# Kernel optimization log

Measured on AMD Instinct MI355X. Metric: run time of the kernel, lower is better.

Reference implementation:

```python
import jax, jax.numpy as jnp
import numpy as np

NEG = float(-2**32 + 1)
LN_EPS = 1e-5

def setup_inputs() -> dict:
    key = jax.random.key(0)
    ks = jax.random.split(key, 10)
    B, Sq, Sk, D = 8, 1024, 1024, 1024
    memory = jax.random.normal(ks[0], (B, Sk, D), jnp.float32)
    decoder_input = jax.random.normal(ks[1], (B, Sq, D), jnp.float32)
    query_mask = jax.random.uniform(ks[2], (B, Sq), jnp.float32)
    Wk = jax.random.normal(ks[3], (D, D), jnp.float32) * 0.02
    Wv = jax.random.normal(ks[4], (D, D), jnp.float32) * 0.02
    Wq = jax.random.normal(ks[5], (D, D), jnp.float32) * 0.02
    Wf = jax.random.normal(ks[6], (2 * D, D), jnp.float32) * 0.02
    bf = jnp.zeros((D,), jnp.float32)
    gamma = jnp.ones((D,), jnp.float32)
    beta = jnp.zeros((D,), jnp.float32)
    mask = jax.random.randint(ks[7], (B, Sq, Sk), 0, 2) == 1
    return dict(memory=memory, decoder_input=decoder_input, query_mask=query_mask,
                Wk=Wk, Wv=Wv, Wq=Wq, Wf=Wf, bf=bf, gamma=gamma, beta=beta, mask=mask)

def reference(memory, decoder_input, query_mask, Wk, Wv, Wq, Wf, bf, gamma, beta, mask):
    B, Sk, D = memory.shape
    Sq = decoder_input.shape[1]
    h = 8
    dh = D // h
    # projections (no bias), split heads -> [h, B, S, dh]
    K = (memory @ Wk).reshape(B, Sk, h, dh).transpose(2, 0, 1, 3)
    V = (memory @ Wv).reshape(B, Sk, h, dh).transpose(2, 0, 1, 3)
    Q = (decoder_input @ Wq).reshape(B, Sq, h, dh).transpose(2, 0, 1, 3)
    # scores [h, B, Sq, Sk]
    attn = jnp.einsum('hbqd,hbkd->hbqk', Q, K) / jnp.sqrt(jnp.float32(dh))
    attn = jnp.where(mask[None], NEG, attn)
    attn = jax.nn.softmax(attn, axis=-1)
    # non-standard post-softmax query-mask multiply
    attn = attn * query_mask[None, :, :, None]
    x = jnp.einsum('hbqk,hbkd->hbqd', attn, V)      # [h,B,Sq,dh]
    x = x.transpose(1, 2, 0, 3).reshape(B, Sq, D)    # concat heads
    x = jnp.concatenate([decoder_input, x], axis=-1)  # [B,Sq,2D]
    x = x @ Wf + bf
    x = x + decoder_input
    # LayerNorm
    mu = jnp.mean(x, axis=-1, keepdims=True)
    var = jnp.var(x, axis=-1, keepdims=True)
    x = (x - mu) * jax.lax.rsqrt(var + LN_EPS) * gamma + beta
    attns = attn.reshape(h * B, Sq, Sk)  # match torch layout [h*B,Sq,Sk]
    return x, attns
```

## Files before the change

kernel.cpp:

```cpp
#include <hip/hip_runtime.h>
#include <hip/hip_bf16.h>
#include <stdint.h>

typedef __attribute__((ext_vector_type(4))) float  floatx4;
typedef __attribute__((ext_vector_type(8))) short  shortx8;

__device__ __forceinline__ unsigned short f2bf(float f) {
    unsigned int u = __builtin_bit_cast(unsigned int, f);
    u += 0x7FFFu + ((u >> 16) & 1u);
    return (unsigned short)(u >> 16);
}
__device__ __forceinline__ float bf2f(unsigned short h) {
    unsigned int u = (unsigned int)h << 16;
    return __builtin_bit_cast(float, u);
}

__device__ __forceinline__ uint4 pack8(float4 a, float4 b) {
    uint4 r;
    r.x = (unsigned)f2bf(a.x) | ((unsigned)f2bf(a.y) << 16);
    r.y = (unsigned)f2bf(a.z) | ((unsigned)f2bf(a.w) << 16);
    r.z = (unsigned)f2bf(b.x) | ((unsigned)f2bf(b.y) << 16);
    r.w = (unsigned)f2bf(b.z) | ((unsigned)f2bf(b.w) << 16);
    return r;
}

__device__ __forceinline__ void gload16(const ushort* g, ushort* l) {
    __builtin_amdgcn_global_load_lds(
        (const __attribute__((address_space(1))) unsigned int*)g,
        (__attribute__((address_space(3))) unsigned int*)l, 16, 0, 0);
}

__global__ __launch_bounds__(256) void cast_both(const float* __restrict__ mem,
                                                 const float* __restrict__ dec,
                                                 ushort* __restrict__ mem_bf,
                                                 ushort* __restrict__ concat) {
    if (blockIdx.x < 4096) {
        long long i = ((long long)blockIdx.x * 256 + threadIdx.x) * 8;
        const float4* p = (const float4*)(mem + i);
        *(uint4*)(mem_bf + i) = pack8(p[0], p[1]);
    } else {
        long long i = ((long long)(blockIdx.x - 4096) * 256 + threadIdx.x) * 8;
        long long r = i >> 10, c = i & 1023;
        const float4* p = (const float4*)(dec + i);
        *(uint4*)(concat + r * 2048 + c) = pack8(p[0], p[1]);
    }
}

__global__ __launch_bounds__(256) void wtrans(const float* __restrict__ W,
                                              ushort* __restrict__ WT, int K, int N) {
    __shared__ float t[32][33];
    int tx = threadIdx.x, ty = threadIdx.y;
    int bx = blockIdx.x * 32;
    int by = blockIdx.y * 32;
    #pragma unroll
    for (int i = 0; i < 4; i++)
        t[ty + 8 * i][tx] = W[(size_t)(by + ty + 8 * i) * N + bx + tx];
    __syncthreads();
    #pragma unroll
    for (int i = 0; i < 4; i++)
        WT[(size_t)(bx + ty + 8 * i) * K + by + tx] = f2bf(t[tx][ty + 8 * i]);
}

__global__ __launch_bounds__(256) void wtrans3(const float* __restrict__ W0,
                                               const float* __restrict__ W1,
                                               const float* __restrict__ W2,
                                               ushort* __restrict__ T0,
                                               ushort* __restrict__ T1,
                                               ushort* __restrict__ T2) {
    __shared__ float t[32][33];
    const float* W = blockIdx.z == 0 ? W0 : (blockIdx.z == 1 ? W1 : W2);
    ushort* WT     = blockIdx.z == 0 ? T0 : (blockIdx.z == 1 ? T1 : T2);
    int tx = threadIdx.x, ty = threadIdx.y;
    int bx = blockIdx.x * 32;
    int by = blockIdx.y * 32;
    #pragma unroll
    for (int i = 0; i < 4; i++)
        t[ty + 8 * i][tx] = W[(size_t)(by + ty + 8 * i) * 1024 + bx + tx];
    __syncthreads();
    #pragma unroll
    for (int i = 0; i < 4; i++)
        WT[(size_t)(bx + ty + 8 * i) * 1024 + by + tx] = f2bf(t[tx][ty + 8 * i]);
}

__global__ __launch_bounds__(256) void vtrans(const ushort* __restrict__ V,
                                              ushort* __restrict__ VT) {
    __shared__ ushort t[32][33];
    int tx = threadIdx.x, ty = threadIdx.y;
    int bk = blockIdx.x * 32;
    int bd = blockIdx.y * 32;
    int z = blockIdx.z;
    int b = z >> 3, h = z & 7;
    #pragma unroll
    for (int i = 0; i < 4; i++)
        t[ty + 8 * i][tx] = V[((size_t)(b * 1024 + bk + ty + 8 * i)) * 1024 + h * 128 + bd + tx];
    __syncthreads();
    #pragma unroll
    for (int i = 0; i < 4; i++)
        VT[((size_t)((h * 8 + b) * 128 + bd + ty + 8 * i)) * 1024 + bk + tx] = t[tx][ty + 8 * i];
}

template <typename TC>
__global__ __launch_bounds__(256) void gemm_bt(
    const ushort* __restrict__ A, const ushort* __restrict__ Bt, TC* __restrict__ C,
    int K, int lda, int ldb, int ldc) {
    __shared__ ushort As[128 * 64];
    __shared__ ushort Bs[128 * 64];

    int tid = threadIdx.x;
    int bm = blockIdx.y * 128, bn = blockIdx.x * 128;
    int l = tid & 63, wid = tid >> 6;
    int l16 = l & 15, quad = l >> 4;
    int wm = (wid & 1) * 64, wn = (wid >> 1) * 64;

    int srow = tid >> 3;
    int scol = (tid & 7) * 8;

    floatx4 acc[4][4];
    #pragma unroll
    for (int i = 0; i < 4; i++)
        #pragma unroll
        for (int j = 0; j < 4; j++)
            acc[i][j] = {0.0f, 0.0f, 0.0f, 0.0f};

    for (int kt = 0; kt < K; kt += 64) {
        #pragma unroll
        for (int it = 0; it < 4; it++) {
            int row = it * 32 + srow;
            gload16(A + (size_t)(bm + row) * lda + kt + scol, &As[row * 64 + scol]);
            gload16(Bt + (size_t)(bn + row) * ldb + kt + scol, &Bs[row * 64 + scol]);
        }
        __syncthreads();
        #pragma unroll
        for (int kk = 0; kk < 64; kk += 32) {
            shortx8 af[4], bfr[4];
            #pragma unroll
            for (int i = 0; i < 4; i++)
                af[i] = *(const shortx8*)&As[(wm + i * 16 + l16) * 64 + kk + quad * 8];
            #pragma unroll
            for (int j = 0; j < 4; j++)
                bfr[j] = *(const shortx8*)&Bs[(wn + j * 16 + l16) * 64 + kk + quad * 8];
            #pragma unroll
            for (int i = 0; i < 4; i++)
                #pragma unroll
                for (int j = 0; j < 4; j++)
                    acc[i][j] = __builtin_amdgcn_mfma_f32_16x16x32_bf16(af[i], bfr[j], acc[i][j], 0, 0, 0);
        }
        __syncthreads();
    }

    #pragma unroll
    for (int i = 0; i < 4; i++) {
        #pragma unroll
        for (int j = 0; j < 4; j++) {
            int row0 = bm + wm + i * 16 + quad * 4;
            int col = bn + wn + j * 16 + l16;
            #pragma unroll
            for (int r = 0; r < 4; r++) {
                float v = acc[i][j][r];
                size_t idx = (size_t)(row0 + r) * ldc + col;
                if constexpr (__is_same(TC, float)) C[idx] = v;
                else C[idx] = f2bf(v);
            }
        }
    }
}

__global__ __launch_bounds__(256) void fused_attn(
    const ushort* __restrict__ Qp, const ushort* __restrict__ Kp,
    const ushort* __restrict__ VT, const int* __restrict__ mask,
    const float* __restrict__ qmask, float* __restrict__ attns,
    ushort* __restrict__ concat) {
    __shared__ ushort Qs[16 * 136];
    __shared__ ushort Ss[16 * 1032];
    __shared__ float rowpart[16][17];
    __shared__ float scale_s[16];

    const int b = blockIdx.z, h = blockIdx.y, q0 = blockIdx.x * 16;
    const int tid = threadIdx.x;
    const int w = tid >> 6, l = tid & 63;
    const int l16 = l & 15, quad = l >> 4;
    const float sc = 0.08838834764831845f;

    {
        int row = tid >> 4, col = (tid & 15) * 8;
        *(uint4*)&Qs[row * 136 + col] =
            *(const uint4*)(Qp + (size_t)(b * 1024 + q0 + row) * 1024 + h * 128 + col);
    }
    __syncthreads();

    shortx8 af[4];
    #pragma unroll
    for (int kk = 0; kk < 4; kk++)
        af[kk] = *(const shortx8*)&Qs[l16 * 136 + kk * 32 + quad * 8];

    const size_t mbase = (size_t)b * 1048576 + (size_t)q0 * 1024;
    for (int c = 0; c < 16; ++c) {
        int k0 = c * 64 + w * 16;
        const ushort* Kr = Kp + (size_t)(b * 1024 + k0 + l16) * 1024 + h * 128 + quad * 8;
        floatx4 acc = {0.0f, 0.0f, 0.0f, 0.0f};
        #pragma unroll
        for (int kk = 0; kk < 4; ++kk)
            acc = __builtin_amdgcn_mfma_f32_16x16x32_bf16(af[kk], *(const shortx8*)(Kr + kk * 32), acc, 0, 0, 0);
        #pragma unroll
        for (int r = 0; r < 4; ++r) {
            int q = quad * 4 + r;
            int m = mask[mbase + (size_t)q * 1024 + k0 + l16];
            float v = m ? 0.0f : __expf(acc[r] * sc);
            Ss[q * 1032 + k0 + l16] = f2bf(v);
        }
    }
    __syncthreads();

    {
        int row = tid >> 4, cs = (tid & 15) * 64;
        float s = 0.0f;
        #pragma unroll
        for (int i = 0; i < 8; ++i) {
            shortx8 v = *(const shortx8*)&Ss[row * 1032 + cs + i * 8];
            #pragma unroll
            for (int j = 0; j < 8; ++j) s += bf2f((unsigned short)v[j]);
        }
        rowpart[row][tid & 15] = s;
    }
    __syncthreads();
    if (tid < 16) {
        float s = 0.0f;
        #pragma unroll
        for (int i = 0; i < 16; ++i) s += rowpart[tid][i];
        scale_s[tid] = qmask[b * 1024 + q0 + tid] / s;
    }
    __syncthreads();

    {
        int row = tid >> 4;
        float scl = scale_s[row];
        float* arow = attns + ((size_t)((h * 8 + b) * 1024 + q0 + row)) * 1024;
        int c0 = (tid & 15) * 4;
        #pragma unroll
        for (int j = 0; j < 16; ++j) {
            int c = c0 + j * 64;
            ushort4 v = *(const ushort4*)&Ss[row * 1032 + c];
            floatx4 o;
            o.x = bf2f(v.x) * scl;
            o.y = bf2f(v.y) * scl;
            o.z = bf2f(v.z) * scl;
            o.w = bf2f(v.w) * scl;
            __builtin_nontemporal_store(o, (floatx4*)(arow + c));
        }
    }

    const size_t vrow0 = (size_t)((h * 8 + b) * 128 + w * 32);
    floatx4 oacc[2] = {{0.0f, 0.0f, 0.0f, 0.0f}, {0.0f, 0.0f, 0.0f, 0.0f}};
    for (int c = 0; c < 16; ++c) {
        #pragma unroll
        for (int ks = 0; ks < 2; ++ks) {
            shortx8 a = *(const shortx8*)&Ss[l16 * 1032 + c * 64 + ks * 32 + quad * 8];
            #pragma unroll
            for (int j = 0; j < 2; ++j) {
                const ushort* vp = VT + (vrow0 + j * 16 + l16) * 1024 + c * 64 + ks * 32 + quad * 8;
                oacc[j] = __builtin_amdgcn_mfma_f32_16x16x32_bf16(a, *(const shortx8*)vp, oacc[j], 0, 0, 0);
            }
        }
    }
    #pragma unroll
    for (int j = 0; j < 2; ++j) {
        #pragma unroll
        for (int r = 0; r < 4; ++r) {
            int q = quad * 4 + r;
            int d = w * 32 + j * 16 + l16;
            float v = oacc[j][r] * scale_s[q];
            concat[(size_t)(b * 1024 + q0 + q) * 2048 + 1024 + h * 128 + d] = f2bf(v);
        }
    }
}

__global__ __launch_bounds__(256) void ln_out(const float* __restrict__ ffn,
                                              const float* __restrict__ dec,
                                              const float* __restrict__ bfv,
                                              const float* __restrict__ gamma,
                                              const float* __restrict__ beta,
                                              float* __restrict__ out) {
    __shared__ float sb[8];
    int row = blockIdx.x, tid = threadIdx.x;
    int c = tid * 4;
    size_t base = (size_t)row * 1024 + c;
    float4 x = *(const float4*)(ffn + base);
    float4 d = *(const float4*)(dec + base);
    float4 bb = *(const float4*)(bfv + c);
    x.x += d.x + bb.x; x.y += d.y + bb.y; x.z += d.z + bb.z; x.w += d.w + bb.w;

    float s = x.x + x.y + x.z + x.w;
    float s2 = x.x * x.x + x.y * x.y + x.z * x.z + x.w * x.w;
    #pragma unroll
    for (int o = 32; o; o >>= 1) {
        s += __shfl_down(s, o, 64);
        s2 += __shfl_down(s2, o, 64);
    }
    if ((tid & 63) == 0) { sb[tid >> 6] = s; sb[4 + (tid >> 6)] = s2; }
    __syncthreads();
    s = sb[0] + sb[1] + sb[2] + sb[3];
    s2 = sb[4] + sb[5] + sb[6] + sb[7];
    float mu = s * (1.0f / 1024.0f);
    float var = s2 * (1.0f / 1024.0f) - mu * mu;
    float rs = rsqrtf(var + 1e-5f);

    float4 g = *(const float4*)(gamma + c);
    float4 be = *(const float4*)(beta + c);
    float4 o4;
    o4.x = (x.x - mu) * rs * g.x + be.x;
    o4.y = (x.y - mu) * rs * g.y + be.y;
    o4.z = (x.z - mu) * rs * g.z + be.z;
    o4.w = (x.w - mu) * rs * g.w + be.w;
    *(float4*)(out + base) = o4;
}

extern "C" void kernel_launch(void* const* d_in, const int* in_sizes, int n_in,
                              void* d_out, int out_size, void* d_ws, size_t ws_size,
                              hipStream_t stream) {
    const float* memory  = (const float*)d_in[0];
    const float* decoder = (const float*)d_in[1];
    const float* qmask   = (const float*)d_in[2];
    const float* Wk      = (const float*)d_in[3];
    const float* Wv      = (const float*)d_in[4];
    const float* Wq      = (const float*)d_in[5];
    const float* Wf      = (const float*)d_in[6];
    const float* bfv     = (const float*)d_in[7];
    const float* gamma   = (const float*)d_in[8];
    const float* beta    = (const float*)d_in[9];
    const int*   mask    = (const int*)d_in[10];

    float* xout  = (float*)d_out;
    float* attns = xout + 8388608LL;

    char* w = (char*)d_ws;
    ushort* mem_bf = (ushort*)(w + 0);
    ushort* Kp     = (ushort*)(w + (16LL << 20));
    float*  ffn    = (float*)(w + 0);
    ushort* Qp     = (ushort*)(w + (32LL << 20));
    ushort* Vp     = (ushort*)(w + (48LL << 20));
    ushort* VT     = (ushort*)(w + (64LL << 20));
    ushort* concat = (ushort*)(w + (80LL << 20));
    ushort* WkT    = (ushort*)(w + (112LL << 20));
    ushort* WvT    = (ushort*)(w + (114LL << 20));
    ushort* WqT    = (ushort*)(w + (116LL << 20));
    ushort* WfT    = (ushort*)(w + (118LL << 20));

    cast_both<<<8192, 256, 0, stream>>>(memory, decoder, mem_bf, concat);
    wtrans3<<<dim3(32, 32, 3), dim3(32, 8), 0, stream>>>(Wk, Wv, Wq, WkT, WvT, WqT);
    wtrans<<<dim3(32, 64), dim3(32, 8), 0, stream>>>(Wf, WfT, 2048, 1024);
    gemm_bt<ushort><<<dim3(8, 64), 256, 0, stream>>>(mem_bf, WkT, Kp, 1024, 1024, 1024, 1024);
    gemm_bt<ushort><<<dim3(8, 64), 256, 0, stream>>>(mem_bf, WvT, Vp, 1024, 1024, 1024, 1024);
    gemm_bt<ushort><<<dim3(8, 64), 256, 0, stream>>>(concat, WqT, Qp, 1024, 2048, 1024, 1024);
    vtrans<<<dim3(32, 4, 64), dim3(32, 8), 0, stream>>>(Vp, VT);
    fused_attn<<<dim3(64, 8, 8), 256, 0, stream>>>(Qp, Kp, VT, mask, qmask, attns, concat);
    gemm_bt<float><<<dim3(8, 64), 256, 0, stream>>>(concat, WfT, ffn, 2048, 2048, 2048, 1024);
    ln_out<<<8192, 256, 0, stream>>>(ffn, decoder, bfv, gamma, beta, xout);
}
```

Baseline: 774.1 us.

## Bit-pack attention mask, merge projection GEMMs, split-K FFN, prefetch K/V in attention

Packs the int32 mask into 64-bit ballot words once, so each attention block reads 16 bits per row pair instead of re-reading int32 mask entries per head. The three projection GEMMs are merged into one launch, and the FFN GEMM is split along K into two partial outputs that LayerNorm sums, doubling the grid for more parallelism. Inside attention, K and V fragments are register-prefetched one chunk ahead, row sums are accumulated during exponentiation instead of by a separate shared-memory pass, and MFMA priority is raised. This costs an extra pack kernel plus an extra fp32 partial buffer read in LayerNorm.

```diff
diff --git a/kernel.cpp b/kernel.cpp
--- a/kernel.cpp
+++ b/kernel.cpp
@@ -46,6 +46,18 @@
     }
 }
 
+__global__ __launch_bounds__(256) void pack_mask(const int* __restrict__ mask,
+                                                 unsigned long long* __restrict__ mb) {
+    int gw = (blockIdx.x * 256 + threadIdx.x) >> 6;
+    int l = threadIdx.x & 63;
+    #pragma unroll
+    for (int i = 0; i < 16; ++i) {
+        size_t widx = (size_t)gw * 16 + i;
+        unsigned long long m = __ballot(mask[widx * 64 + l] != 0);
+        if (l == 0) mb[widx] = m;
+    }
+}
+
 __global__ __launch_bounds__(256) void wtrans(const float* __restrict__ W,
                                               ushort* __restrict__ WT, int K, int N) {
     __shared__ float t[32][33];
@@ -100,18 +112,15 @@
 }
 
 template <typename TC>
-__global__ __launch_bounds__(256) void gemm_bt(
-    const ushort* __restrict__ A, const ushort* __restrict__ Bt, TC* __restrict__ C,
-    int K, int lda, int ldb, int ldc) {
-    __shared__ ushort As[128 * 64];
-    __shared__ ushort Bs[128 * 64];
-
+__device__ __forceinline__ void gemm_core(ushort* As, ushort* Bs,
+                                          const ushort* __restrict__ A,
+                                          const ushort* __restrict__ Bt, TC* __restrict__ C,
+                                          int kbeg, int kend, int lda, int ldb, int ldc,
+                                          int bm, int bn) {
     int tid = threadIdx.x;
-    int bm = blockIdx.y * 128, bn = blockIdx.x * 128;
     int l = tid & 63, wid = tid >> 6;
     int l16 = l & 15, quad = l >> 4;
     int wm = (wid & 1) * 64, wn = (wid >> 1) * 64;
-
     int srow = tid >> 3;
     int scol = (tid & 7) * 8;
 
@@ -122,7 +131,7 @@
         for (int j = 0; j < 4; j++)
             acc[i][j] = {0.0f, 0.0f, 0.0f, 0.0f};
 
-    for (int kt = 0; kt < K; kt += 64) {
+    for (int kt = kbeg; kt < kend; kt += 64) {
         #pragma unroll
         for (int it = 0; it < 4; it++) {
             int row = it * 32 + srow;
@@ -165,14 +174,41 @@
     }
 }
 
-__global__ __launch_bounds__(256) void fused_attn(
+__global__ __launch_bounds__(256) void gemm_proj3(
+    const ushort* __restrict__ mem_bf, const ushort* __restrict__ concat,
+    const ushort* __restrict__ WkT, const ushort* __restrict__ WvT,
+    const ushort* __restrict__ WqT,
+    ushort* __restrict__ Kp, ushort* __restrict__ Vp, ushort* __restrict__ Qp) {
+    __shared__ ushort As[128 * 64];
+    __shared__ ushort Bs[128 * 64];
+    const ushort* A; const ushort* Bt; ushort* C; int lda;
+    if (blockIdx.z == 0)      { A = mem_bf; Bt = WkT; C = Kp; lda = 1024; }
+    else if (blockIdx.z == 1) { A = mem_bf; Bt = WvT; C = Vp; lda = 1024; }
+    else                      { A = concat; Bt = WqT; C = Qp; lda = 2048; }
+    gemm_core<ushort>(As, Bs, A, Bt, C, 0, 1024, lda, 1024, 1024,
+                      blockIdx.y * 128, blockIdx.x * 128);
+}
+
+__global__ __launch_bounds__(256) void gemm_ffn(
+    const ushort* __restrict__ concat, const ushort* __restrict__ WfT,
+    float* __restrict__ ffn0, float* __restrict__ ffn1) {
+    __shared__ ushort As[128 * 64];
+    __shared__ ushort Bs[128 * 64];
+    int z = blockIdx.z;
+    gemm_core<float>(As, Bs, concat, WfT, z ? ffn1 : ffn0,
+                     z * 1024, z * 1024 + 1024, 2048, 2048, 1024,
+                     blockIdx.y * 128, blockIdx.x * 128);
+}
+
+__global__ __launch_bounds__(256, 4) void fused_attn(
     const ushort* __restrict__ Qp, const ushort* __restrict__ Kp,
-    const ushort* __restrict__ VT, const int* __restrict__ mask,
+    const ushort* __restrict__ VT, const unsigned long long* __restrict__ mb,
     const float* __restrict__ qmask, float* __restrict__ attns,
     ushort* __restrict__ concat) {
     __shared__ ushort Qs[16 * 136];
     __shared__ ushort Ss[16 * 1032];
-    __shared__ float rowpart[16][17];
+    __shared__ unsigned Ms[16][34];
+    __shared__ float rowpart[16][5];
     __shared__ float scale_s[16];
 
     const int b = blockIdx.z, h = blockIdx.y, q0 = blockIdx.x * 16;
@@ -185,6 +221,10 @@
         int row = tid >> 4, col = (tid & 15) * 8;
         *(uint4*)&Qs[row * 136 + col] =
             *(const uint4*)(Qp + (size_t)(b * 1024 + q0 + row) * 1024 + h * 128 + col);
+        int pr = tid & 15;
+        uint2 mv = ((const uint2*)mb)[(size_t)(b * 1024 + q0 + row) * 16 + pr];
+        Ms[row][pr * 2] = mv.x;
+        Ms[row][pr * 2 + 1] = mv.y;
     }
     __syncthreads();
 
@@ -193,40 +233,54 @@
     for (int kk = 0; kk < 4; kk++)
         af[kk] = *(const shortx8*)&Qs[l16 * 136 + kk * 32 + quad * 8];
 
-    const size_t mbase = (size_t)b * 1048576 + (size_t)q0 * 1024;
+    const ushort* Kb = Kp + (size_t)(b * 1024 + w * 16 + l16) * 1024 + h * 128 + quad * 8;
+    shortx8 kf0 = *(const shortx8*)(Kb + 0);
+    shortx8 kf1 = *(const shortx8*)(Kb + 32);
+    shortx8 kf2 = *(const shortx8*)(Kb + 64);
+    shortx8 kf3 = *(const shortx8*)(Kb + 96);
+    float ssum[4] = {0.0f, 0.0f, 0.0f, 0.0f};
+    const int bp64 = w * 16 + l16;
+    const int wsel = bp64 >> 5, bitp = bp64 & 31;
     for (int c = 0; c < 16; ++c) {
+        int cn = c < 15 ? c + 1 : c;
+        const ushort* Kn = Kb + (size_t)cn * 65536;
+        shortx8 kn0 = *(const shortx8*)(Kn + 0);
+        shortx8 kn1 = *(const shortx8*)(Kn + 32);
+        shortx8 kn2 = *(const shortx8*)(Kn + 64);
+        shortx8 kn3 = *(const shortx8*)(Kn + 96);
+        floatx4 acc = {0.0f, 0.0f, 0.0f, 0.0f};
+        __builtin_amdgcn_s_setprio(1);
+        acc = __builtin_amdgcn_mfma_f32_16x16x32_bf16(af[0], kf0, acc, 0, 0, 0);
+        acc = __builtin_amdgcn_mfma_f32_16x16x32_bf16(af[1], kf1, acc, 0, 0, 0);
+        acc = __builtin_amdgcn_mfma_f32_16x16x32_bf16(af[2], kf2, acc, 0, 0, 0);
+        acc = __builtin_amdgcn_mfma_f32_16x16x32_bf16(af[3], kf3, acc, 0, 0, 0);
+        __builtin_amdgcn_s_setprio(0);
         int k0 = c * 64 + w * 16;
-        const ushort* Kr = Kp + (size_t)(b * 1024 + k0 + l16) * 1024 + h * 128 + quad * 8;
-        floatx4 acc = {0.0f, 0.0f, 0.0f, 0.0f};
-        #pragma unroll
-        for (int kk = 0; kk < 4; ++kk)
-            acc = __builtin_amdgcn_mfma_f32_16x16x32_bf16(af[kk], *(const shortx8*)(Kr + kk * 32), acc, 0, 0, 0);
         #pragma unroll
         for (int r = 0; r < 4; ++r) {
             int q = quad * 4 + r;
-            int m = mask[mbase + (size_t)q * 1024 + k0 + l16];
-            float v = m ? 0.0f : __expf(acc[r] * sc);
+            unsigned wv = Ms[q][c * 2 + wsel];
+            float v = ((wv >> bitp) & 1u) ? 0.0f : __expf(acc[r] * sc);
+            ssum[r] += v;
             Ss[q * 1032 + k0 + l16] = f2bf(v);
         }
-    }
-    __syncthreads();
-
-    {
-        int row = tid >> 4, cs = (tid & 15) * 64;
-        float s = 0.0f;
-        #pragma unroll
-        for (int i = 0; i < 8; ++i) {
-            shortx8 v = *(const shortx8*)&Ss[row * 1032 + cs + i * 8];
-            #pragma unroll
-            for (int j = 0; j < 8; ++j) s += bf2f((unsigned short)v[j]);
-        }
-        rowpart[row][tid & 15] = s;
+        kf0 = kn0; kf1 = kn1; kf2 = kn2; kf3 = kn3;
+    }
+
+    #pragma unroll
+    for (int r = 0; r < 4; ++r) {
+        float s = ssum[r];
+        #pragma unroll
+        for (int off = 1; off < 16; off <<= 1) s += __shfl_xor(s, off, 16);
+        ssum[r] = s;
+    }
+    if (l16 == 0) {
+        #pragma unroll
+        for (int r = 0; r < 4; ++r) rowpart[quad * 4 + r][w] = ssum[r];
     }
     __syncthreads();
     if (tid < 16) {
-        float s = 0.0f;
-        #pragma unroll
-        for (int i = 0; i < 16; ++i) s += rowpart[tid][i];
+        float s = rowpart[tid][0] + rowpart[tid][1] + rowpart[tid][2] + rowpart[tid][3];
         scale_s[tid] = qmask[b * 1024 + q0 + tid] / s;
     }
     __syncthreads();
@@ -250,31 +304,42 @@
     }
 
     const size_t vrow0 = (size_t)((h * 8 + b) * 128 + w * 32);
-    floatx4 oacc[2] = {{0.0f, 0.0f, 0.0f, 0.0f}, {0.0f, 0.0f, 0.0f, 0.0f}};
+    const ushort* Vb0 = VT + (vrow0 + l16) * 1024 + quad * 8;
+    const ushort* Vb1 = VT + (vrow0 + 16 + l16) * 1024 + quad * 8;
+    shortx8 v00 = *(const shortx8*)(Vb0);
+    shortx8 v01 = *(const shortx8*)(Vb1);
+    shortx8 v10 = *(const shortx8*)(Vb0 + 32);
+    shortx8 v11 = *(const shortx8*)(Vb1 + 32);
+    floatx4 o0 = {0.0f, 0.0f, 0.0f, 0.0f}, o1 = {0.0f, 0.0f, 0.0f, 0.0f};
     for (int c = 0; c < 16; ++c) {
-        #pragma unroll
-        for (int ks = 0; ks < 2; ++ks) {
-            shortx8 a = *(const shortx8*)&Ss[l16 * 1032 + c * 64 + ks * 32 + quad * 8];
-            #pragma unroll
-            for (int j = 0; j < 2; ++j) {
-                const ushort* vp = VT + (vrow0 + j * 16 + l16) * 1024 + c * 64 + ks * 32 + quad * 8;
-                oacc[j] = __builtin_amdgcn_mfma_f32_16x16x32_bf16(a, *(const shortx8*)vp, oacc[j], 0, 0, 0);
-            }
-        }
-    }
-    #pragma unroll
-    for (int j = 0; j < 2; ++j) {
-        #pragma unroll
-        for (int r = 0; r < 4; ++r) {
-            int q = quad * 4 + r;
-            int d = w * 32 + j * 16 + l16;
-            float v = oacc[j][r] * scale_s[q];
-            concat[(size_t)(b * 1024 + q0 + q) * 2048 + 1024 + h * 128 + d] = f2bf(v);
-        }
-    }
-}
-
-__global__ __launch_bounds__(256) void ln_out(const float* __restrict__ ffn,
+        int cn = c < 15 ? c + 1 : c;
+        shortx8 n00 = *(const shortx8*)(Vb0 + cn * 64);
+        shortx8 n01 = *(const shortx8*)(Vb1 + cn * 64);
+        shortx8 n10 = *(const shortx8*)(Vb0 + cn * 64 + 32);
+        shortx8 n11 = *(const shortx8*)(Vb1 + cn * 64 + 32);
+        shortx8 pa0 = *(const shortx8*)&Ss[l16 * 1032 + c * 64 + quad * 8];
+        shortx8 pa1 = *(const shortx8*)&Ss[l16 * 1032 + c * 64 + 32 + quad * 8];
+        __builtin_amdgcn_s_setprio(1);
+        o0 = __builtin_amdgcn_mfma_f32_16x16x32_bf16(pa0, v00, o0, 0, 0, 0);
+        o1 = __builtin_amdgcn_mfma_f32_16x16x32_bf16(pa0, v01, o1, 0, 0, 0);
+        o0 = __builtin_amdgcn_mfma_f32_16x16x32_bf16(pa1, v10, o0, 0, 0, 0);
+        o1 = __builtin_amdgcn_mfma_f32_16x16x32_bf16(pa1, v11, o1, 0, 0, 0);
+        __builtin_amdgcn_s_setprio(0);
+        v00 = n00; v01 = n01; v10 = n10; v11 = n11;
+    }
+    #pragma unroll
+    for (int r = 0; r < 4; ++r) {
+        int q = quad * 4 + r;
+        float scl = scale_s[q];
+        int d = w * 32 + l16;
+        size_t base = (size_t)(b * 1024 + q0 + q) * 2048 + 1024 + h * 128;
+        concat[base + d]      = f2bf(o0[r] * scl);
+        concat[base + d + 16] = f2bf(o1[r] * scl);
+    }
+}
+
+__global__ __launch_bounds__(256) void ln_out(const float* __restrict__ ffn0,
+                                              const float* __restrict__ ffn1,
                                               const float* __restrict__ dec,
                                               const float* __restrict__ bfv,
                                               const float* __restrict__ gamma,
@@ -284,10 +349,12 @@
     int row = blockIdx.x, tid = threadIdx.x;
     int c = tid * 4;
     size_t base = (size_t)row * 1024 + c;
-    float4 x = *(const float4*)(ffn + base);
+    float4 x = *(const float4*)(ffn0 + base);
+    float4 y = *(const float4*)(ffn1 + base);
     float4 d = *(const float4*)(dec + base);
     float4 bb = *(const float4*)(bfv + c);
-    x.x += d.x + bb.x; x.y += d.y + bb.y; x.z += d.z + bb.z; x.w += d.w + bb.w;
+    x.x += y.x + d.x + bb.x; x.y += y.y + d.y + bb.y;
+    x.z += y.z + d.z + bb.z; x.w += y.w + d.w + bb.w;
 
     float s = x.x + x.y + x.z + x.w;
     float s2 = x.x * x.x + x.y * x.y + x.z * x.z + x.w * x.w;
@@ -335,7 +402,6 @@
     char* w = (char*)d_ws;
     ushort* mem_bf = (ushort*)(w + 0);
     ushort* Kp     = (ushort*)(w + (16LL << 20));
-    float*  ffn    = (float*)(w + 0);
     ushort* Qp     = (ushort*)(w + (32LL << 20));
     ushort* Vp     = (ushort*)(w + (48LL << 20));
     ushort* VT     = (ushort*)(w + (64LL << 20));
@@ -344,15 +410,17 @@
     ushort* WvT    = (ushort*)(w + (114LL << 20));
     ushort* WqT    = (ushort*)(w + (116LL << 20));
     ushort* WfT    = (ushort*)(w + (118LL << 20));
+    unsigned long long* mbits = (unsigned long long*)(w + (48LL << 20));
+    float* ffn0 = (float*)(w + 0);
+    float* ffn1 = (float*)(w + (32LL << 20));
 
     cast_both<<<8192, 256, 0, stream>>>(memory, decoder, mem_bf, concat);
     wtrans3<<<dim3(32, 32, 3), dim3(32, 8), 0, stream>>>(Wk, Wv, Wq, WkT, WvT, WqT);
     wtrans<<<dim3(32, 64), dim3(32, 8), 0, stream>>>(Wf, WfT, 2048, 1024);
-    gemm_bt<ushort><<<dim3(8, 64), 256, 0, stream>>>(mem_bf, WkT, Kp, 1024, 1024, 1024, 1024);
-    gemm_bt<ushort><<<dim3(8, 64), 256, 0, stream>>>(mem_bf, WvT, Vp, 1024, 1024, 1024, 1024);
-    gemm_bt<ushort><<<dim3(8, 64), 256, 0, stream>>>(concat, WqT, Qp, 1024, 2048, 1024, 1024);
+    gemm_proj3<<<dim3(8, 64, 3), 256, 0, stream>>>(mem_bf, concat, WkT, WvT, WqT, Kp, Vp, Qp);
     vtrans<<<dim3(32, 4, 64), dim3(32, 8), 0, stream>>>(Vp, VT);
-    fused_attn<<<dim3(64, 8, 8), 256, 0, stream>>>(Qp, Kp, VT, mask, qmask, attns, concat);
-    gemm_bt<float><<<dim3(8, 64), 256, 0, stream>>>(concat, WfT, ffn, 2048, 2048, 2048, 1024);
-    ln_out<<<8192, 256, 0, stream>>>(ffn, decoder, bfv, gamma, beta, xout);
-}
+    pack_mask<<<2048, 256, 0, stream>>>(mask, mbits);
+    fused_attn<<<dim3(64, 8, 8), 256, 0, stream>>>(Qp, Kp, VT, mbits, qmask, attns, concat);
+    gemm_ffn<<<dim3(8, 64, 2), 256, 0, stream>>>(concat, WfT, ffn0, ffn1);
+    ln_out<<<8192, 256, 0, stream>>>(ffn0, ffn1, decoder, bfv, gamma, beta, xout);
+}
```

Result: faster. 752.4 us (-2.8%).
